# Kernel optimization log

Hardware: AMD Instinct MI355X
Metric: run time of the kernel (lower is better)

## Reference

```python
import jax, jax.numpy as jnp
import numpy as np


def gcn_conv(x, W, b, src, dst, num_nodes):
    """PyG GCNConv with add_self_loops=True, symmetric normalization, bias.
    src/dst already include self-loops. deg computed from unit edge weights."""
    deg = jax.ops.segment_sum(jnp.ones(src.shape[0], x.dtype), dst,
                              num_segments=num_nodes)
    dinv = jnp.where(deg > 0, jax.lax.rsqrt(deg), 0.0)
    norm = dinv[src] * dinv[dst]               # [E]
    h = x @ W                                  # [N, F_out] dense GEMM first
    msg = h[src] * norm[:, None]               # gather + scale, [E, F_out]
    out = jax.ops.segment_sum(msg, dst, num_segments=num_nodes)  # scatter-add
    return out + b


def setup_inputs() -> dict:
    key = jax.random.key(0)
    ks = jax.random.split(key, 5)
    N, E, F_in, F_out = 50000, 800000, 512, 40
    x = jax.random.normal(ks[0], (N, F_in), dtype=jnp.float32)
    edge_index = jax.random.randint(ks[1], (2, E), 0, N, dtype=jnp.int64)
    W1 = jax.random.normal(ks[2], (F_in, 256), dtype=jnp.float32) * (F_in ** -0.5)
    W2 = jax.random.normal(ks[3], (256, 16), dtype=jnp.float32) * (256 ** -0.5)
    W3 = jax.random.normal(ks[4], (16, F_out), dtype=jnp.float32) * (16 ** -0.5)
    return {
        "x": x, "edge_index": edge_index,
        "W1": W1, "b1": jnp.zeros((256,), jnp.float32),
        "W2": W2, "b2": jnp.zeros((16,), jnp.float32),
        "W3": W3, "b3": jnp.zeros((F_out,), jnp.float32),
    }


def reference(x, edge_index, W1, b1, W2, b2, W3, b3):
    N = x.shape[0]
    loop = jnp.arange(N, dtype=edge_index.dtype)
    src = jnp.concatenate([edge_index[0], loop])  # self-loops appended once,
    dst = jnp.concatenate([edge_index[1], loop])  # shared by all three layers
    h = gcn_conv(x, W1, b1, src, dst, N)
    h = jax.nn.relu(h)                 # dropout is identity in eval mode
    h = gcn_conv(h, W2, b2, src, dst, N)
    h = jax.nn.relu(h)
    h = gcn_conv(h, W3, b3, src, dst, N)
    return jax.nn.log_softmax(h, axis=1)
```

## Files before the change

kernel.cpp:

```cpp
#include <hip/hip_runtime.h>
#include <hip/hip_bf16.h>
#include <math.h>

typedef __hip_bfloat16 bf16;
typedef __attribute__((ext_vector_type(8))) __bf16 bf16x8;
typedef __attribute__((ext_vector_type(4))) float f32x4;

#define KIN 512
#define F1  256
#define F2  16
#define F3  40


__device__ inline unsigned pk_bf2(float a, float b) {
  bf16 x = __float2bfloat16(a), y = __float2bfloat16(b);
  unsigned short ux = *(unsigned short*)&x, uy = *(unsigned short*)&y;
  return (unsigned)ux | ((unsigned)uy << 16);
}
__device__ inline float bfbits(unsigned u16) {
  unsigned v = u16 << 16;
  return *(float*)&v;
}
__device__ inline void async16(const void* g, void* l) {
  __builtin_amdgcn_global_load_lds((const __attribute__((address_space(1))) void*)g,
                                   (__attribute__((address_space(3))) void*)l, 16, 0, 0);
}
__device__ inline void accum8(float* acc, uint4 h, float w) {
  acc[0] = fmaf(w, bfbits(h.x & 0xffff), acc[0]);
  acc[1] = fmaf(w, bfbits(h.x >> 16),    acc[1]);
  acc[2] = fmaf(w, bfbits(h.y & 0xffff), acc[2]);
  acc[3] = fmaf(w, bfbits(h.y >> 16),    acc[3]);
  acc[4] = fmaf(w, bfbits(h.z & 0xffff), acc[4]);
  acc[5] = fmaf(w, bfbits(h.z >> 16),    acc[5]);
  acc[6] = fmaf(w, bfbits(h.w & 0xffff), acc[6]);
  acc[7] = fmaf(w, bfbits(h.w >> 16),    acc[7]);
}


__global__ __launch_bounds__(256) void k_init2(int* __restrict__ cnt,
                                               const int* __restrict__ ei, int* __restrict__ flag,
                                               const float* __restrict__ W,
                                               unsigned short* __restrict__ Wt,
                                               int n, int nb) {
  int b = blockIdx.x;
  int t = threadIdx.x;
  if (b < nb) {
    int i = b * 256 + t;
    if (i < n) cnt[i] = 0;
    if (b == 0 && t == 0)
      *flag = (ei[1] == 0 && ei[3] == 0 && ei[5] == 0 && ei[7] == 0) ? 1 : 0;
  } else {
    __shared__ float tile[32][33];
    int b2 = b - nb;
    int k0 = (b2 & 15) * 32;
    int n0 = (b2 >> 4) * 32;
    int lr = t >> 5, lc = t & 31;
#pragma unroll
    for (int rr = 0; rr < 32; rr += 8)
      tile[lr + rr][lc] = W[(size_t)(k0 + lr + rr) * F1 + n0 + lc];
    __syncthreads();
#pragma unroll
    for (int rr = 0; rr < 32; rr += 8) {
      bf16 v = __float2bfloat16(tile[lc][lr + rr]);
      Wt[(size_t)(n0 + lr + rr) * KIN + k0 + lc] = *(unsigned short*)&v;
    }
  }
}


__global__ __launch_bounds__(256) void k_count_conv(const int* __restrict__ ei,
                                                    const int* __restrict__ flag,
                                                    int* __restrict__ cnt,
                                                    int* __restrict__ rank,
                                                    int E, int nct, int stride,
                                                    const float* __restrict__ X,
                                                    unsigned short* __restrict__ Xb,
                                                    int total8) {
  int b = blockIdx.x;
  int t = threadIdx.x;
  bool is_cnt = (b % stride == 0) && (b / stride < nct);
  if (is_cnt) {
    int e = (b / stride) * 256 + t;
    if (e >= E) return;
    int is64 = *flag;
    int d = is64 ? ei[2 * E + 2 * e] : ei[E + e];
    rank[e] = atomicAdd(&cnt[d], 1);
  } else {
    int nb_before = (b + stride - 1) / stride;
    if (nb_before > nct) nb_before = nct;
    int idx = (b - nb_before) * 256 + t;
    if (idx >= total8) return;
    const float4* src = (const float4*)X + (size_t)idx * 2;
    float4 f0 = src[0], f1 = src[1];
    uint4 pk;
    pk.x = pk_bf2(f0.x, f0.y); pk.y = pk_bf2(f0.z, f0.w);
    pk.z = pk_bf2(f1.x, f1.y); pk.w = pk_bf2(f1.z, f1.w);
    ((uint4*)Xb)[idx] = pk;
  }
}

__global__ __launch_bounds__(256) void k_scan1(const int* __restrict__ cnt,
                                               int* __restrict__ off,
                                               int* __restrict__ bsum,
                                               float* __restrict__ dinv, int N) {
  __shared__ int s[256];
  int t = threadIdx.x;
  int base = blockIdx.x * 1024 + t * 4;
  int v0 = (base + 0 < N) ? cnt[base + 0] : 0;
  int v1 = (base + 1 < N) ? cnt[base + 1] : 0;
  int v2 = (base + 2 < N) ? cnt[base + 2] : 0;
  int v3 = (base + 3 < N) ? cnt[base + 3] : 0;
  if (base + 0 < N) dinv[base + 0] = rsqrtf((float)(v0 + 1));
  if (base + 1 < N) dinv[base + 1] = rsqrtf((float)(v1 + 1));
  if (base + 2 < N) dinv[base + 2] = rsqrtf((float)(v2 + 1));
  if (base + 3 < N) dinv[base + 3] = rsqrtf((float)(v3 + 1));
  int tsum = v0 + v1 + v2 + v3;
  s[t] = tsum;
  __syncthreads();
  for (int d = 1; d < 256; d <<= 1) {
    int u = (t >= d) ? s[t - d] : 0;
    __syncthreads();
    s[t] += u;
    __syncthreads();
  }
  int excl = s[t] - tsum;
  int p0 = excl + v0, p1 = p0 + v1, p2 = p1 + v2, p3 = p2 + v3;
  if (base + 0 < N) off[base + 1] = p0;
  if (base + 1 < N) off[base + 2] = p1;
  if (base + 2 < N) off[base + 3] = p2;
  if (base + 3 < N) off[base + 4] = p3;
  if (t == 255) bsum[blockIdx.x] = s[255];
}

__global__ __launch_bounds__(256) void k_scan3m(int* __restrict__ off,
                                                const int* __restrict__ bsum, int N) {
  __shared__ int cs;
  int t = threadIdx.x;
  if (t < 64) {
    int v = (t < blockIdx.x) ? bsum[t] : 0;
    for (int d = 32; d; d >>= 1) v += __shfl_xor(v, d, 64);
    if (t == 0) cs = v;
  }
  __syncthreads();
  int c = cs;
  int base = blockIdx.x * 1024 + t * 4;
#pragma unroll
  for (int k = 0; k < 4; ++k)
    if (base + k < N) off[base + k + 1] += c;
  if (blockIdx.x == 0 && t == 0) off[0] = 0;
}


__global__ __launch_bounds__(256) void k_gemm1_sc(const unsigned short* __restrict__ Ab,
                                                  const unsigned short* __restrict__ Bt,
                                                  bf16* __restrict__ C, int M, int ngx,
                                                  const int* __restrict__ ei,
                                                  const int* __restrict__ flag,
                                                  const int* __restrict__ off,
                                                  const int* __restrict__ rank,
                                                  const float* __restrict__ dinv,
                                                  int2* __restrict__ ew, int E) {
  __shared__ unsigned short As[128 * 32];
  __shared__ unsigned short Bs[128 * 32];
  int b = blockIdx.x;
  int t = threadIdx.x;
  int ngemm = ngx * 2;
  if (b >= ngemm) {
    int e = (b - ngemm) * 256 + t;
    if (e >= E) return;
    int is64 = *flag;
    int s, d;
    if (is64) { s = ei[2 * e]; d = ei[2 * E + 2 * e]; }
    else      { s = ei[e];     d = ei[E + e]; }
    int pos = off[d] + rank[e];
    float w = dinv[s] * dinv[d];
    ew[pos] = make_int2(s, __float_as_int(w));
    return;
  }
  int wave = t >> 6, lane = t & 63;
  int wm = wave >> 1, wn = wave & 1;
  int row0 = (b % ngx) * 128, col0 = (b / ngx) * 128;
  int q = lane >> 4, m16 = lane & 15;
  int srow = lane >> 2, schk = lane & 3;

  f32x4 acc[4][4];
#pragma unroll
  for (int i = 0; i < 4; ++i)
#pragma unroll
    for (int j = 0; j < 4; ++j) acc[i][j] = {0.f, 0.f, 0.f, 0.f};

  for (int kb = 0; kb < 16; ++kb) {
    __syncthreads();
#pragma unroll
    for (int jj = 0; jj < 2; ++jj) {
      int lr = wave * 32 + jj * 16 + srow;
      int gr = row0 + lr; if (gr >= M) gr = M - 1;
      int gchk = schk ^ ((lr >> 1) & 3);
      async16(Ab + (size_t)gr * KIN + kb * 32 + gchk * 8,
              As + (wave * 32 + jj * 16) * 32);
    }
#pragma unroll
    for (int jj = 0; jj < 2; ++jj) {
      int lr = wave * 32 + jj * 16 + srow;
      int gchk = schk ^ ((lr >> 1) & 3);
      async16(Bt + (size_t)(col0 + lr) * KIN + kb * 32 + gchk * 8,
              Bs + (wave * 32 + jj * 16) * 32);
    }
    __syncthreads();
    bf16x8 af[4], bfr[4];
#pragma unroll
    for (int i = 0; i < 4; ++i) {
      int m = wm * 64 + i * 16 + m16;
      af[i] = *(const bf16x8*)(As + m * 32 + ((q ^ ((m >> 1) & 3)) * 8));
    }
#pragma unroll
    for (int j = 0; j < 4; ++j) {
      int n = wn * 64 + j * 16 + m16;
      bfr[j] = *(const bf16x8*)(Bs + n * 32 + ((q ^ ((n >> 1) & 3)) * 8));
    }
#pragma unroll
    for (int j = 0; j < 4; ++j)
#pragma unroll
      for (int i = 0; i < 4; ++i)
        acc[i][j] = __builtin_amdgcn_mfma_f32_16x16x32_bf16(af[i], bfr[j], acc[i][j], 0, 0, 0);
  }

#pragma unroll
  for (int i = 0; i < 4; ++i) {
#pragma unroll
    for (int r = 0; r < 4; ++r) {
      int row = row0 + wm * 64 + i * 16 + q * 4 + r;
      if (row < M) {
#pragma unroll
        for (int j = 0; j < 4; ++j) {
          int col = col0 + wn * 64 + j * 16 + m16;
          C[(size_t)row * F1 + col] = __float2bfloat16(acc[i][j][r]);
        }
      }
    }
  }
}


__global__ __launch_bounds__(256) void k_agg1(const bf16* __restrict__ H,
                                              const int* __restrict__ off,
                                              const int2* __restrict__ ew,
                                              const float* __restrict__ dinv,
                                              const float* __restrict__ bias,
                                              bf16* __restrict__ O, int N, int nbb) {
  int b = blockIdx.x;
  int t = threadIdx.x;
  int phase = (b >= nbb) ? 1 : 0;
  int b2 = b - phase * nbb;
  int i = b2 * 16 + (t >> 4);
  if (i >= N) return;
  int f0 = phase * 128 + (t & 15) * 8;
  const unsigned short* Hu = (const unsigned short*)H;
  float di = dinv[i];
  float w0 = di * di;
  float acc[8];
  {
    uint4 h = *(const uint4*)(Hu + (size_t)i * F1 + f0);
    acc[0] = w0 * bfbits(h.x & 0xffff); acc[1] = w0 * bfbits(h.x >> 16);
    acc[2] = w0 * bfbits(h.y & 0xffff); acc[3] = w0 * bfbits(h.y >> 16);
    acc[4] = w0 * bfbits(h.z & 0xffff); acc[5] = w0 * bfbits(h.z >> 16);
    acc[6] = w0 * bfbits(h.w & 0xffff); acc[7] = w0 * bfbits(h.w >> 16);
  }
  int e = off[i], e1 = off[i + 1];
  for (; e + 8 <= e1; e += 8) {
    int2 p0 = ew[e + 0], p1 = ew[e + 1], p2 = ew[e + 2], p3 = ew[e + 3];
    int2 p4 = ew[e + 4], p5 = ew[e + 5], p6 = ew[e + 6], p7 = ew[e + 7];
    uint4 g0 = *(const uint4*)(Hu + (size_t)p0.x * F1 + f0);
    uint4 g1 = *(const uint4*)(Hu + (size_t)p1.x * F1 + f0);
    uint4 g2 = *(const uint4*)(Hu + (size_t)p2.x * F1 + f0);
    uint4 g3 = *(const uint4*)(Hu + (size_t)p3.x * F1 + f0);
    uint4 g4 = *(const uint4*)(Hu + (size_t)p4.x * F1 + f0);
    uint4 g5 = *(const uint4*)(Hu + (size_t)p5.x * F1 + f0);
    uint4 g6 = *(const uint4*)(Hu + (size_t)p6.x * F1 + f0);
    uint4 g7 = *(const uint4*)(Hu + (size_t)p7.x * F1 + f0);
    accum8(acc, g0, __int_as_float(p0.y));
    accum8(acc, g1, __int_as_float(p1.y));
    accum8(acc, g2, __int_as_float(p2.y));
    accum8(acc, g3, __int_as_float(p3.y));
    accum8(acc, g4, __int_as_float(p4.y));
    accum8(acc, g5, __int_as_float(p5.y));
    accum8(acc, g6, __int_as_float(p6.y));
    accum8(acc, g7, __int_as_float(p7.y));
  }
  for (; e < e1; ++e) {
    int2 pe = ew[e];
    uint4 g = *(const uint4*)(Hu + (size_t)pe.x * F1 + f0);
    accum8(acc, g, __int_as_float(pe.y));
  }
  float4 b0 = *(const float4*)(bias + f0);
  float4 b1 = *(const float4*)(bias + f0 + 4);
  float bb[8] = {b0.x, b0.y, b0.z, b0.w, b1.x, b1.y, b1.z, b1.w};
  uint4 o;
  unsigned* op = (unsigned*)&o;
#pragma unroll
  for (int k = 0; k < 4; ++k) {
    float lo = fmaxf(acc[2 * k] + bb[2 * k], 0.f);
    float hi = fmaxf(acc[2 * k + 1] + bb[2 * k + 1], 0.f);
    op[k] = pk_bf2(lo, hi);
  }
  *(uint4*)((unsigned short*)O + (size_t)i * F1 + f0) = o;
}


__global__ __launch_bounds__(256) void k_gemm2(const bf16* __restrict__ A,
                                               const float* __restrict__ W,
                                               float* __restrict__ C, int N) {
  __shared__ float Ws[F1 * F2];
  __shared__ float Ts[16][F1];
  int t = threadIdx.x;
  int r0 = blockIdx.x * 16;
#pragma unroll
  for (int j = 0; j < 16; ++j) Ws[t + 256 * j] = W[t + 256 * j];
  const unsigned short* Au = (const unsigned short*)A;
#pragma unroll
  for (int j = 0; j < 2; ++j) {
    int idx = t + 256 * j;
    int r = idx >> 5;
    int c8 = (idx & 31) * 8;
    int row = r0 + r;
    uint4 g = make_uint4(0, 0, 0, 0);
    if (row < N) g = *(const uint4*)(Au + (size_t)row * F1 + c8);
    float* ts = &Ts[r][c8];
    ts[0] = bfbits(g.x & 0xffff); ts[1] = bfbits(g.x >> 16);
    ts[2] = bfbits(g.y & 0xffff); ts[3] = bfbits(g.y >> 16);
    ts[4] = bfbits(g.z & 0xffff); ts[5] = bfbits(g.z >> 16);
    ts[6] = bfbits(g.w & 0xffff); ts[7] = bfbits(g.w >> 16);
  }
  __syncthreads();
  int r = t >> 4, c = t & 15;
  float acc = 0.f;
  const float4* tv = (const float4*)&Ts[r][0];
#pragma unroll 8
  for (int k4 = 0; k4 < 64; ++k4) {
    float4 a = tv[k4];
    int k = k4 * 4;
    acc = fmaf(a.x, Ws[(k + 0) * 16 + c], acc);
    acc = fmaf(a.y, Ws[(k + 1) * 16 + c], acc);
    acc = fmaf(a.z, Ws[(k + 2) * 16 + c], acc);
    acc = fmaf(a.w, Ws[(k + 3) * 16 + c], acc);
  }
  int row = r0 + r;
  if (row < N) C[(size_t)row * F2 + c] = acc;
}


__global__ __launch_bounds__(256) void k_agg16(const float* __restrict__ H,
                                               const int* __restrict__ off,
                                               const int2* __restrict__ ew,
                                               const float* __restrict__ dinv,
                                               const float* __restrict__ bias,
                                               float* __restrict__ O, int N) {
  int t = threadIdx.x;
  int i = blockIdx.x * 16 + (t >> 4);
  int f = t & 15;
  if (i >= N) return;
  float di = dinv[i];
  float acc = di * di * H[(size_t)i * F2 + f];
  int e = off[i], e1 = off[i + 1];
  for (; e + 4 <= e1; e += 4) {
    int2 p0 = ew[e + 0], p1 = ew[e + 1], p2 = ew[e + 2], p3 = ew[e + 3];
    float g0 = H[(size_t)p0.x * F2 + f];
    float g1 = H[(size_t)p1.x * F2 + f];
    float g2 = H[(size_t)p2.x * F2 + f];
    float g3 = H[(size_t)p3.x * F2 + f];
    acc = fmaf(__int_as_float(p0.y), g0, acc);
    acc = fmaf(__int_as_float(p1.y), g1, acc);
    acc = fmaf(__int_as_float(p2.y), g2, acc);
    acc = fmaf(__int_as_float(p3.y), g3, acc);
  }
  for (; e < e1; ++e) {
    int2 pe = ew[e];
    acc = fmaf(__int_as_float(pe.y), H[(size_t)pe.x * F2 + f], acc);
  }
  acc = fmaxf(acc + bias[f], 0.f);
  O[(size_t)i * F2 + f] = acc;
}


__global__ __launch_bounds__(256) void k_agg3_g3(const float* __restrict__ H,
                                                 const int* __restrict__ off,
                                                 const int2* __restrict__ ew,
                                                 const float* __restrict__ dinv,
                                                 const float* __restrict__ W3,
                                                 const float* __restrict__ b3,
                                                 float* __restrict__ O, int N) {
  __shared__ float W3s[F2 * F3];
  __shared__ float b3s[F3];
  __shared__ float aggs[16 * 17];
  int t = threadIdx.x;
  for (int idx = t; idx < F2 * F3; idx += 256) W3s[idx] = W3[idx];
  if (t < F3) b3s[t] = b3[t];
  __syncthreads();

  int node = t >> 4, f = t & 15;
  int i = blockIdx.x * 16 + node;
  if (i >= N) return;
  float di = dinv[i];
  float acc = di * di * H[(size_t)i * F2 + f];
  int e = off[i], e1 = off[i + 1];
  for (; e + 4 <= e1; e += 4) {
    int2 p0 = ew[e + 0], p1 = ew[e + 1], p2 = ew[e + 2], p3 = ew[e + 3];
    float g0 = H[(size_t)p0.x * F2 + f];
    float g1 = H[(size_t)p1.x * F2 + f];
    float g2 = H[(size_t)p2.x * F2 + f];
    float g3 = H[(size_t)p3.x * F2 + f];
    acc = fmaf(__int_as_float(p0.y), g0, acc);
    acc = fmaf(__int_as_float(p1.y), g1, acc);
    acc = fmaf(__int_as_float(p2.y), g2, acc);
    acc = fmaf(__int_as_float(p3.y), g3, acc);
  }
  for (; e < e1; ++e) {
    int2 pe = ew[e];
    acc = fmaf(__int_as_float(pe.y), H[(size_t)pe.x * F2 + f], acc);
  }
  aggs[node * 17 + f] = acc;

  const float* ar = &aggs[node * 17];
  float o0 = b3s[f], o1 = b3s[f + 16], o2 = (f < 8) ? b3s[f + 32] : 0.f;
#pragma unroll
  for (int k = 0; k < F2; ++k) {
    float a = ar[k];
    o0 = fmaf(a, W3s[k * F3 + f], o0);
    o1 = fmaf(a, W3s[k * F3 + f + 16], o1);
    if (f < 8) o2 = fmaf(a, W3s[k * F3 + f + 32], o2);
  }
  float m = fmaxf(o0, o1);
  if (f < 8) m = fmaxf(m, o2);
#pragma unroll
  for (int d = 1; d < 16; d <<= 1) m = fmaxf(m, __shfl_xor(m, d, 16));
  float s = __expf(o0 - m) + __expf(o1 - m) + ((f < 8) ? __expf(o2 - m) : 0.f);
#pragma unroll
  for (int d = 1; d < 16; d <<= 1) s += __shfl_xor(s, d, 16);
  float lse = m + __logf(s);
  float* orow = O + (size_t)i * F3;
  orow[f] = o0 - lse;
  orow[f + 16] = o1 - lse;
  if (f < 8) orow[f + 32] = o2 - lse;
}


extern "C" void kernel_launch(void* const* d_in, const int* in_sizes, int n_in,
                              void* d_out, int out_size, void* d_ws, size_t ws_size,
                              hipStream_t stream) {
  const float* x  = (const float*)d_in[0];
  const int*   ei = (const int*)d_in[1];
  const float* W1 = (const float*)d_in[2];
  const float* b1 = (const float*)d_in[3];
  const float* W2 = (const float*)d_in[4];
  const float* b2 = (const float*)d_in[5];
  const float* W3 = (const float*)d_in[6];
  const float* b3 = (const float*)d_in[7];
  float* out = (float*)d_out;

  int N = in_sizes[0] / KIN;
  int E = in_sizes[1] / 2;

  char* p = (char*)d_ws;
  auto take = [&](size_t bytes) {
    char* r = p;
    p += (bytes + 255) & ~(size_t)255;
    return r;
  };
  int*   flag  = (int*)take(4);
  int*   cnt   = (int*)take((size_t)N * 4);
  int*   off   = (int*)take((size_t)(N + 1) * 4);
  float* dinv  = (float*)take((size_t)N * 4);
  int*   bsum  = (int*)take(64 * 4);
  int*   rank  = (int*)take((size_t)E * 4);
  int2*  ew    = (int2*)take((size_t)E * 8);
  unsigned short* w1t = (unsigned short*)take((size_t)KIN * F1 * 2);
  unsigned short* xb  = (unsigned short*)take((size_t)N * KIN * 2);
  bf16*  h1    = (bf16*)take((size_t)N * F1 * 2);
  bf16*  out1  = (bf16*)take((size_t)N * F1 * 2);
  float* h2    = (float*)take((size_t)N * F2 * 4);
  float* out2  = (float*)take((size_t)N * F2 * 4);

  int nb  = (N + 255) / 256;
  int ebk = (E + 255) / 256;
  int nsc = (N + 1023) / 1024;
  int total8 = (N * KIN) / 8;
  int cvb = (total8 + 255) / 256;
  int tot = ebk + cvb;
  int stride = tot / ebk; if (stride < 1) stride = 1;

  k_init2<<<nb + 128, 256, 0, stream>>>(cnt, ei, flag, W1, w1t, N, nb);
  k_count_conv<<<tot, 256, 0, stream>>>(ei, flag, cnt, rank, E, ebk, stride, x, xb, total8);
  k_scan1<<<nsc, 256, 0, stream>>>(cnt, off, bsum, dinv, N);
  k_scan3m<<<nsc, 256, 0, stream>>>(off, bsum, N);

  int ngx = (N + 127) / 128;
  k_gemm1_sc<<<ngx * 2 + ebk, 256, 0, stream>>>(xb, w1t, h1, N, ngx,
                                                ei, flag, off, rank, dinv, ew, E);

  int nbb = (N + 15) / 16;
  k_agg1<<<nbb * 2, 256, 0, stream>>>(h1, off, ew, dinv, b1, out1, N, nbb);
  k_gemm2<<<(N + 15) / 16, 256, 0, stream>>>(out1, W2, h2, N);
  k_agg16<<<(N + 15) / 16, 256, 0, stream>>>(h2, off, ew, dinv, b2, out2, N);
  k_agg3_g3<<<(N + 15) / 16, 256, 0, stream>>>(out2, off, ew, dinv, W3, b3, out, N);
}
```

Baseline: 347.1 us.

## Sort nodes by in-degree bins to balance aggregation work per block

Builds a 64-bin histogram of node in-degrees during the scan and prefix-sums it. Extra blocks in the GEMM1 launch then emit a permutation that groups nodes by degree. All three aggregation kernels process nodes in that order, so the 16 nodes in a block have similar edge counts and lanes diverge less. In exchange, each aggregation adds an indirection through perm, output writes and self-row reads become scattered, and ordering inside a bin depends on atomics.

```diff
diff --git a/kernel.cpp b/kernel.cpp
--- a/kernel.cpp
+++ b/kernel.cpp
@@ -10,6 +10,7 @@
 #define F1  256
 #define F2  16
 #define F3  40
+#define NBIN 64
 
 
 __device__ inline unsigned pk_bf2(float a, float b) {
@@ -41,12 +42,14 @@
                                                const int* __restrict__ ei, int* __restrict__ flag,
                                                const float* __restrict__ W,
                                                unsigned short* __restrict__ Wt,
+                                               int* __restrict__ hist,
                                                int n, int nb) {
   int b = blockIdx.x;
   int t = threadIdx.x;
   if (b < nb) {
     int i = b * 256 + t;
     if (i < n) cnt[i] = 0;
+    if (b == 0 && t < NBIN) hist[t] = 0;
     if (b == 0 && t == 0)
       *flag = (ei[1] == 0 && ei[3] == 0 && ei[5] == 0 && ei[7] == 0) ? 1 : 0;
   } else {
@@ -102,9 +105,12 @@
 __global__ __launch_bounds__(256) void k_scan1(const int* __restrict__ cnt,
                                                int* __restrict__ off,
                                                int* __restrict__ bsum,
-                                               float* __restrict__ dinv, int N) {
+                                               float* __restrict__ dinv,
+                                               int* __restrict__ hist, int N) {
   __shared__ int s[256];
-  int t = threadIdx.x;
+  __shared__ int lh[NBIN];
+  int t = threadIdx.x;
+  if (t < NBIN) lh[t] = 0;
   int base = blockIdx.x * 1024 + t * 4;
   int v0 = (base + 0 < N) ? cnt[base + 0] : 0;
   int v1 = (base + 1 < N) ? cnt[base + 1] : 0;
@@ -117,6 +123,10 @@
   int tsum = v0 + v1 + v2 + v3;
   s[t] = tsum;
   __syncthreads();
+  if (base + 0 < N) atomicAdd(&lh[v0 < 63 ? v0 : 63], 1);
+  if (base + 1 < N) atomicAdd(&lh[v1 < 63 ? v1 : 63], 1);
+  if (base + 2 < N) atomicAdd(&lh[v2 < 63 ? v2 : 63], 1);
+  if (base + 3 < N) atomicAdd(&lh[v3 < 63 ? v3 : 63], 1);
   for (int d = 1; d < 256; d <<= 1) {
     int u = (t >= d) ? s[t - d] : 0;
     __syncthreads();
@@ -130,16 +140,27 @@
   if (base + 2 < N) off[base + 3] = p2;
   if (base + 3 < N) off[base + 4] = p3;
   if (t == 255) bsum[blockIdx.x] = s[255];
+  if (t < NBIN) {
+    int h = lh[t];
+    if (h) atomicAdd(&hist[t], h);
+  }
 }
 
 __global__ __launch_bounds__(256) void k_scan3m(int* __restrict__ off,
-                                                const int* __restrict__ bsum, int N) {
+                                                const int* __restrict__ bsum,
+                                                const int* __restrict__ hist,
+                                                int* __restrict__ binoff, int N) {
   __shared__ int cs;
   int t = threadIdx.x;
   if (t < 64) {
     int v = (t < blockIdx.x) ? bsum[t] : 0;
     for (int d = 32; d; d >>= 1) v += __shfl_xor(v, d, 64);
     if (t == 0) cs = v;
+  }
+  if (blockIdx.x == 0 && t < NBIN) {
+    int a = 0;
+    for (int j = 0; j < t; ++j) a += hist[j];
+    binoff[t] = a;
   }
   __syncthreads();
   int c = cs;
@@ -159,12 +180,33 @@
                                                   const int* __restrict__ off,
                                                   const int* __restrict__ rank,
                                                   const float* __restrict__ dinv,
-                                                  int2* __restrict__ ew, int E) {
+                                                  int2* __restrict__ ew, int E, int ebk,
+                                                  const int* __restrict__ cnt,
+                                                  int* __restrict__ binoff,
+                                                  int* __restrict__ perm) {
   __shared__ unsigned short As[128 * 32];
   __shared__ unsigned short Bs[128 * 32];
+  __shared__ int lh[NBIN], lb[NBIN];
   int b = blockIdx.x;
   int t = threadIdx.x;
   int ngemm = ngx * 2;
+  if (b >= ngemm + ebk) {
+    int idx = (b - ngemm - ebk) * 256 + t;
+    if (t < NBIN) lh[t] = 0;
+    __syncthreads();
+    int bin = 0, lr2 = 0;
+    bool valid = (idx < M);
+    if (valid) {
+      int d = cnt[idx];
+      bin = d < 63 ? d : 63;
+      lr2 = atomicAdd(&lh[bin], 1);
+    }
+    __syncthreads();
+    if (t < NBIN && lh[t] > 0) lb[t] = atomicAdd(&binoff[t], lh[t]);
+    __syncthreads();
+    if (valid) perm[lb[bin] + lr2] = idx;
+    return;
+  }
   if (b >= ngemm) {
     int e = (b - ngemm) * 256 + t;
     if (e >= E) return;
@@ -247,13 +289,15 @@
                                               const int2* __restrict__ ew,
                                               const float* __restrict__ dinv,
                                               const float* __restrict__ bias,
+                                              const int* __restrict__ perm,
                                               bf16* __restrict__ O, int N, int nbb) {
   int b = blockIdx.x;
   int t = threadIdx.x;
   int phase = (b >= nbb) ? 1 : 0;
   int b2 = b - phase * nbb;
-  int i = b2 * 16 + (t >> 4);
-  if (i >= N) return;
+  int idx = b2 * 16 + (t >> 4);
+  if (idx >= N) return;
+  int i = perm[idx];
   int f0 = phase * 128 + (t & 15) * 8;
   const unsigned short* Hu = (const unsigned short*)H;
   float di = dinv[i];
@@ -354,11 +398,13 @@
                                                const int2* __restrict__ ew,
                                                const float* __restrict__ dinv,
                                                const float* __restrict__ bias,
+                                               const int* __restrict__ perm,
                                                float* __restrict__ O, int N) {
   int t = threadIdx.x;
-  int i = blockIdx.x * 16 + (t >> 4);
+  int idx = blockIdx.x * 16 + (t >> 4);
   int f = t & 15;
-  if (i >= N) return;
+  if (idx >= N) return;
+  int i = perm[idx];
   float di = dinv[i];
   float acc = di * di * H[(size_t)i * F2 + f];
   int e = off[i], e1 = off[i + 1];
@@ -388,18 +434,20 @@
                                                  const float* __restrict__ dinv,
                                                  const float* __restrict__ W3,
                                                  const float* __restrict__ b3,
+                                                 const int* __restrict__ perm,
                                                  float* __restrict__ O, int N) {
   __shared__ float W3s[F2 * F3];
   __shared__ float b3s[F3];
   __shared__ float aggs[16 * 17];
   int t = threadIdx.x;
-  for (int idx = t; idx < F2 * F3; idx += 256) W3s[idx] = W3[idx];
+  for (int idx2 = t; idx2 < F2 * F3; idx2 += 256) W3s[idx2] = W3[idx2];
   if (t < F3) b3s[t] = b3[t];
   __syncthreads();
 
   int node = t >> 4, f = t & 15;
-  int i = blockIdx.x * 16 + node;
-  if (i >= N) return;
+  int idx = blockIdx.x * 16 + node;
+  if (idx >= N) return;
+  int i = perm[idx];
   float di = dinv[i];
   float acc = di * di * H[(size_t)i * F2 + f];
   int e = off[i], e1 = off[i + 1];
@@ -471,6 +519,9 @@
   int*   off   = (int*)take((size_t)(N + 1) * 4);
   float* dinv  = (float*)take((size_t)N * 4);
   int*   bsum  = (int*)take(64 * 4);
+  int*   hist  = (int*)take(NBIN * 4);
+  int*   binoff= (int*)take(NBIN * 4);
+  int*   perm  = (int*)take((size_t)N * 4);
   int*   rank  = (int*)take((size_t)E * 4);
   int2*  ew    = (int2*)take((size_t)E * 8);
   unsigned short* w1t = (unsigned short*)take((size_t)KIN * F1 * 2);
@@ -488,18 +539,19 @@
   int tot = ebk + cvb;
   int stride = tot / ebk; if (stride < 1) stride = 1;
 
-  k_init2<<<nb + 128, 256, 0, stream>>>(cnt, ei, flag, W1, w1t, N, nb);
+  k_init2<<<nb + 128, 256, 0, stream>>>(cnt, ei, flag, W1, w1t, hist, N, nb);
   k_count_conv<<<tot, 256, 0, stream>>>(ei, flag, cnt, rank, E, ebk, stride, x, xb, total8);
-  k_scan1<<<nsc, 256, 0, stream>>>(cnt, off, bsum, dinv, N);
-  k_scan3m<<<nsc, 256, 0, stream>>>(off, bsum, N);
+  k_scan1<<<nsc, 256, 0, stream>>>(cnt, off, bsum, dinv, hist, N);
+  k_scan3m<<<nsc, 256, 0, stream>>>(off, bsum, hist, binoff, N);
 
   int ngx = (N + 127) / 128;
-  k_gemm1_sc<<<ngx * 2 + ebk, 256, 0, stream>>>(xb, w1t, h1, N, ngx,
-                                                ei, flag, off, rank, dinv, ew, E);
+  k_gemm1_sc<<<ngx * 2 + ebk + nb, 256, 0, stream>>>(xb, w1t, h1, N, ngx,
+                                                     ei, flag, off, rank, dinv, ew, E, ebk,
+                                                     cnt, binoff, perm);
 
   int nbb = (N + 15) / 16;
-  k_agg1<<<nbb * 2, 256, 0, stream>>>(h1, off, ew, dinv, b1, out1, N, nbb);
+  k_agg1<<<nbb * 2, 256, 0, stream>>>(h1, off, ew, dinv, b1, perm, out1, N, nbb);
   k_gemm2<<<(N + 15) / 16, 256, 0, stream>>>(out1, W2, h2, N);
-  k_agg16<<<(N + 15) / 16, 256, 0, stream>>>(h2, off, ew, dinv, b2, out2, N);
-  k_agg3_g3<<<(N + 15) / 16, 256, 0, stream>>>(out2, off, ew, dinv, W3, b3, out, N);
-}
+  k_agg16<<<(N + 15) / 16, 256, 0, stream>>>(h2, off, ew, dinv, b2, perm, out2, N);
+  k_agg3_g3<<<(N + 15) / 16, 256, 0, stream>>>(out2, off, ew, dinv, W3, b3, perm, out, N);
+}
```

New measurement: 348.3 us. Within noise of the previous version (+0.3%).
